# Optimization experiments

Measured on AMD Instinct MI355X. Metric: run time of the kernel, lower is better.

Reference implementation:

```python
import jax, jax.numpy as jnp
import numpy as np

B, C, H, W = 8, 192, 56, 56
OUT, K = 192, 9
BN_EPS = 1e-5


def _l2_normalize(x, axis):
    # matches torch F.normalize: x / max(||x||, eps)
    n = jnp.sqrt(jnp.sum(x * x, axis=axis, keepdims=True))
    return x / jnp.maximum(n, 1e-12)


def _knn_idx(x_bnc, k):
    # dense pairwise squared distances, then k nearest (includes self)
    sq = jnp.sum(x_bnc * x_bnc, axis=-1, keepdims=True)            # (b,n,1)
    dist = sq - 2.0 * jnp.einsum('bnc,bmc->bnm', x_bnc, x_bnc) + jnp.swapaxes(sq, 1, 2)
    _, idx = jax.lax.top_k(-dist, k)                                # (b,n,k)
    return idx


def setup_inputs() -> dict:
    key = jax.random.key(0)
    k1, k2 = jax.random.split(key)
    fan_in = 2 * C
    return {
        'x': jax.random.normal(k1, (B, C, H, W), dtype=jnp.float32),
        'conv_w': jax.random.normal(k2, (OUT, 2 * C), dtype=jnp.float32) * np.sqrt(2.0 / fan_in),
        'conv_b': jnp.zeros((OUT,), dtype=jnp.float32),
        'bn_gamma': jnp.ones((OUT,), dtype=jnp.float32),
        'bn_beta': jnp.zeros((OUT,), dtype=jnp.float32),
    }


def reference(x, conv_w, conv_b, bn_gamma, bn_beta):
    b, c, h, w = x.shape
    n = h * w
    xf = x.reshape(b, c, n)                      # (b,c,n) node features
    xt = jnp.swapaxes(xf, 1, 2)                  # (b,n,c)

    # graph build on L2-normalized features (torch does this under no_grad)
    xn = _l2_normalize(xt, axis=-1)
    idx = _knn_idx(jax.lax.stop_gradient(xn), K)  # (b,n,K) neighbor ids

    # gather neighbors; center gather is identity (center_idx == arange)
    x_j = jnp.take_along_axis(xt[:, :, None, :], idx[..., None], axis=1)  # (b,n,K,c)
    x_i = xt[:, :, None, :]                                               # (b,n,1,c)
    feat = jnp.concatenate([jnp.broadcast_to(x_i, x_j.shape), x_j - x_i], axis=-1)  # (b,n,K,2c)

    # 1x1 conv == per-edge linear
    y = jnp.einsum('bnke,oe->bnko', feat, conv_w) + conv_b                # (b,n,K,out)

    # BatchNorm2d (training-mode batch stats over b,n,K per channel)
    mean = jnp.mean(y, axis=(0, 1, 2))
    var = jnp.var(y, axis=(0, 1, 2))
    y = (y - mean) * jax.lax.rsqrt(var + BN_EPS) * bn_gamma + bn_beta

    y = jax.nn.gelu(y, approximate=False)
    y = jnp.max(y, axis=2)                        # max over K neighbors -> (b,n,out)
    return jnp.transpose(y, (0, 2, 1)).reshape(b, -1, h, w)
```

## Files before the change

kernel.cpp:

```cpp
#include <hip/hip_runtime.h>
#include <hip/hip_bf16.h>
#include <math.h>

#define BB 8
#define CC 192
#define HH 56
#define WW 56
#define NPTS 3136
#define OUTC 192
#define KNN 9
#define NTILES 49
#define NCH 2
#define NT4 98
#define NBLK4 (NT4 * BB)
#define K2BLKS (BB * NCH * NTILES)
#define K3BLKS ((BB * NPTS / 64) * 6)

typedef __bf16 bf16x8 __attribute__((ext_vector_type(8)));
typedef float  f32x16 __attribute__((ext_vector_type(16)));
typedef int    i32x4  __attribute__((ext_vector_type(4)));

__device__ __forceinline__ unsigned short f2bf(float f) {
    unsigned u = __float_as_uint(f);
    u += 0x7fffu + ((u >> 16) & 1u);
    return (unsigned short)(u >> 16);
}
__device__ __forceinline__ float bf2f(unsigned short h) {
    return __uint_as_float(((unsigned)h) << 16);
}
__device__ __forceinline__ float gelu_f(float z) {
    return 0.5f * z * (1.0f + erff(z * 0.70710678118654752f));
}

__device__ __forceinline__ void ins12u32(unsigned (&t)[12], unsigned key) {
    if (key >= t[11]) return;
    t[11] = key;
#pragma unroll
    for (int q = 11; q > 0; --q) {
        const unsigned a = t[q-1], bq = t[q];
        const bool sw = bq < a;
        t[q-1] = sw ? bq : a;
        t[q]   = sw ? a : bq;
    }
}

__device__ __forceinline__ void ins12u(unsigned long long (&t)[12], unsigned long long key) {
    if (key >= t[11]) return;
    t[11] = key;
#pragma unroll
    for (int q = 11; q > 0; --q) {
        const unsigned long long a = t[q-1], bq = t[q];
        const bool sw = bq < a;
        t[q-1] = sw ? bq : a;
        t[q]   = sw ? a : bq;
    }
}

__device__ __forceinline__ void ins9f(float (&d)[9], int (&ix)[9], float nd, int ni) {
    if (!((nd < d[8]) || (nd == d[8] && ni < ix[8]))) return;
    d[8] = nd; ix[8] = ni;
#pragma unroll
    for (int q = 8; q > 0; --q) {
        if ((d[q] < d[q-1]) || (d[q] == d[q-1] && ix[q] < ix[q-1])) {
            float t = d[q]; d[q] = d[q-1]; d[q-1] = t;
            int t2 = ix[q]; ix[q] = ix[q-1]; ix[q-1] = t2;
        }
    }
}

__global__ __launch_bounds__(256) void k1_normalize(const float* __restrict__ x,
                                                    float* __restrict__ xn,
                                                    unsigned short* __restrict__ xh,
                                                    unsigned short* __restrict__ xl,
                                                    float* __restrict__ normv,
                                                    float* __restrict__ sqv) {
    const int b  = blockIdx.y;
    const int n0 = blockIdx.x * 64;
    __shared__ float tile[64 * 193];
    __shared__ float red[4][64];
    __shared__ float inv[64];
    const int tid = threadIdx.x;
    const int p   = tid & 63;
    const int cg  = tid >> 6;
    const float* xb = x + (size_t)b * CC * NPTS;

    float acc = 0.f;
#pragma unroll 4
    for (int t = 0; t < 48; ++t) {
        const int c = cg * 48 + t;
        const float v = xb[(size_t)c * NPTS + n0 + p];
        tile[p * 193 + c] = v;
        acc += v * v;
    }
    red[cg][p] = acc;
    __syncthreads();
    if (cg == 0) {
        const float s  = red[0][p] + red[1][p] + red[2][p] + red[3][p];
        float nc = sqrtf(s);
        nc = fmaxf(nc, 1e-12f);
        normv[b * NPTS + n0 + p] = nc;
        const float iv = 1.0f / nc;
        inv[p] = iv;
        sqv[b * NPTS + n0 + p] = s * iv * iv;
    }
    __syncthreads();
    const size_t base = ((size_t)b * NPTS + n0) * CC;
    float* dst = xn + base;
    for (int q = tid; q < 64 * CC / 4; q += 256) {
        const int f   = q * 4;
        const int row = f / CC;
        const int c   = f - row * CC;
        const float iv = inv[row];
        float4 v;
        v.x = tile[row * 193 + c + 0] * iv;
        v.y = tile[row * 193 + c + 1] * iv;
        v.z = tile[row * 193 + c + 2] * iv;
        v.w = tile[row * 193 + c + 3] * iv;
        *(float4*)&dst[f] = v;
        ushort4 hv, lv;
        hv.x = f2bf(v.x); lv.x = f2bf(v.x - bf2f(hv.x));
        hv.y = f2bf(v.y); lv.y = f2bf(v.y - bf2f(hv.y));
        hv.z = f2bf(v.z); lv.z = f2bf(v.z - bf2f(hv.z));
        hv.w = f2bf(v.w); lv.w = f2bf(v.w - bf2f(hv.w));
        *(ushort4*)&xh[base + f] = hv;
        *(ushort4*)&xl[base + f] = lv;
    }
}

__global__ __launch_bounds__(256, 3) void k23_mega(const unsigned short* __restrict__ xh,
                                                   const unsigned short* __restrict__ xl,
                                                   unsigned long long* __restrict__ pd,
                                                   const unsigned short* __restrict__ wh,
                                                   const unsigned short* __restrict__ wl,
                                                   const float* __restrict__ normv,
                                                   const float* __restrict__ conv_b,
                                                   float* __restrict__ uv) {
    __shared__ __align__(16) char smem[51200];
    const int bid = blockIdx.x;
    const int tid = threadIdx.x;
    const int w    = tid >> 6;
    const int lane = tid & 63;
    const int l31  = lane & 31;
    const int lhi  = lane >> 5;
    const int koffe = lhi * 8;

    if (bid < K2BLKS) {
        const int b     = bid & 7;
        const int chunk = (bid >> 3) & 1;
        const int r0    = (bid >> 4) * 64;
        const int t0    = chunk ? 25 : 0;
        const int t1    = chunk ? 49 : 25;

        unsigned short* Cs  = (unsigned short*)smem;
        unsigned short* Rk1 = (unsigned short*)(smem + 25600);
        unsigned long long* cdu = (unsigned long long*)smem;

        const int wc   = w & 1;
        const int wr   = w >> 1;
        const int myrow = wc * 32 + l31;
        const int spnt = tid >> 2;
        const int sj   = tid & 3;

        const size_t rbase = ((size_t)b * NPTS + (r0 + myrow)) * CC;
        bf16x8 Rh0[6], Rl0[6];
#pragma unroll
        for (int c = 0; c < 6; ++c) {
            Rh0[c] = *(const bf16x8*)(const void*)(xh + rbase + c * 16 + koffe);
            Rl0[c] = *(const bf16x8*)(const void*)(xl + rbase + c * 16 + koffe);
        }

        {
            const size_t pb = ((size_t)b * NPTS + r0 + spnt) * CC + 96;
#pragma unroll
            for (int rep = 0; rep < 3; ++rep) {
                const int j = sj + rep * 4;
                *(uint4*)(void*)&Rk1[spnt * 200 + j * 8] =
                    *(const uint4*)(const void*)(xh + pb + j * 8);
            }
#pragma unroll
            for (int rep = 0; rep < 3; ++rep) {
                const int j = sj + rep * 4;
                *(uint4*)(void*)&Rk1[spnt * 200 + 96 + j * 8] =
                    *(const uint4*)(const void*)(xl + pb + j * 8);
            }
        }

        unsigned t12[12];
#pragma unroll
        for (int q = 0; q < 12; ++q) t12[q] = 0xFFFFFFFFu;

        const int cfb = (wr * 32 + l31) * 200 + koffe;
        const int rlb = myrow * 200 + koffe;

        for (int ct = t0; ct < t1; ++ct) {
            const int c0 = ct * 64;
            __syncthreads();
            {
                const size_t pb = ((size_t)b * NPTS + c0 + spnt) * CC;
#pragma unroll
                for (int rep = 0; rep < 6; ++rep) {
                    const int j = sj + rep * 4;
                    *(uint4*)(void*)&Cs[spnt * 200 + j * 8] =
                        *(const uint4*)(const void*)(xh + pb + j * 8);
                }
            }
            __syncthreads();

            f32x16 acc;
#pragma unroll
            for (int r = 0; r < 16; ++r) acc[r] = 0.f;

#pragma unroll
            for (int c = 0; c < 6; ++c) {
                const bf16x8 cf = *(const bf16x8*)(const void*)&Cs[cfb + c * 16];
                acc = __builtin_amdgcn_mfma_f32_32x32x16_bf16(cf, Rh0[c], acc, 0, 0, 0);
                acc = __builtin_amdgcn_mfma_f32_32x32x16_bf16(cf, Rl0[c], acc, 0, 0, 0);
            }
#pragma unroll
            for (int c = 0; c < 6; ++c) {
                const bf16x8 cf = *(const bf16x8*)(const void*)&Cs[cfb + (6 + c) * 16];
                const i32x4 th = *(const volatile i32x4*)(const volatile void*)&Rk1[rlb + c * 16];
                const i32x4 tl = *(const volatile i32x4*)(const volatile void*)&Rk1[rlb + 96 + c * 16];
                acc = __builtin_amdgcn_mfma_f32_32x32x16_bf16(cf, __builtin_bit_cast(bf16x8, th), acc, 0, 0, 0);
                acc = __builtin_amdgcn_mfma_f32_32x32x16_bf16(cf, __builtin_bit_cast(bf16x8, tl), acc, 0, 0, 0);
            }
            __syncthreads();
            {
                const size_t pb = ((size_t)b * NPTS + c0 + spnt) * CC;
#pragma unroll
                for (int rep = 0; rep < 6; ++rep) {
                    const int j = sj + rep * 4;
                    *(uint4*)(void*)&Cs[spnt * 200 + j * 8] =
                        *(const uint4*)(const void*)(xl + pb + j * 8);
                }
            }
            __syncthreads();
#pragma unroll
            for (int c = 0; c < 6; ++c) {
                const bf16x8 cl = *(const bf16x8*)(const void*)&Cs[cfb + c * 16];
                acc = __builtin_amdgcn_mfma_f32_32x32x16_bf16(cl, Rh0[c], acc, 0, 0, 0);
            }
#pragma unroll
            for (int c = 0; c < 6; ++c) {
                const bf16x8 cl = *(const bf16x8*)(const void*)&Cs[cfb + (6 + c) * 16];
                const i32x4 th = *(const volatile i32x4*)(const volatile void*)&Rk1[rlb + c * 16];
                acc = __builtin_amdgcn_mfma_f32_32x32x16_bf16(cl, __builtin_bit_cast(bf16x8, th), acc, 0, 0, 0);
            }

            const unsigned tbase = (unsigned)((ct - t0) << 4);
#pragma unroll
            for (int reg = 0; reg < 16; ++reg) {
                const float d = fmaxf(1.0f - acc[reg], 0.0f);
                const unsigned key = (__float_as_uint(d) & 0xFFFFFE00u) | (tbase | (unsigned)reg);
                ins12u32(t12, key);
            }
        }

        __syncthreads();
#pragma unroll
        for (int q = 0; q < 12; ++q) {
            const unsigned key = t12[q];
            const int tag = (int)(key & 511u);
            const int reg = tag & 15;
            const int col = (t0 + (tag >> 4)) * 64 + wr * 32 + ((reg & 3) + 8 * (reg >> 2) + 4 * lhi);
            cdu[(((wr * 2 + lhi) * 64) + myrow) * 12 + q] = ((unsigned long long)key << 32) | (unsigned)col;
        }
        __syncthreads();
        if (tid < 64) {
            unsigned long long t[12];
#pragma unroll
            for (int q = 0; q < 12; ++q) t[q] = cdu[tid * 12 + q];
            for (int s = 1; s < 4; ++s)
#pragma unroll
                for (int q = 0; q < 12; ++q) ins12u(t, cdu[(s * 64 + tid) * 12 + q]);
            const size_t gbase = ((size_t)b * NPTS + r0 + tid) * (NCH * 12) + chunk * 12;
#pragma unroll
            for (int q = 0; q < 12; ++q) pd[gbase + q] = t[q];
        }
    } else {
        const int id2 = bid - K2BLKS;
        const int ot  = id2 % 6;
        const int mt  = id2 / 6;
        const int m0  = mt * 64;
        const int o0  = ot * 64;
        const int wr  = w >> 1;
        const int wc  = w & 1;

        const size_t abase = (size_t)(m0 + wr * 32 + l31) * CC;
        bf16x8 Ah[12], Al[12];
#pragma unroll
        for (int c = 0; c < 12; ++c) {
            Ah[c] = *(const bf16x8*)(const void*)(xh + abase + c * 16 + koffe);
            Al[c] = *(const bf16x8*)(const void*)(xl + abase + c * 16 + koffe);
        }
        const int o = o0 + wc * 32 + l31;
        const unsigned short* whr = wh + (size_t)o * CC;
        const unsigned short* wlr = wl + (size_t)o * CC;

        f32x16 acc;
#pragma unroll
        for (int r = 0; r < 16; ++r) acc[r] = 0.f;
#pragma unroll
        for (int c = 0; c < 12; ++c) {
            const bf16x8 bh = *(const bf16x8*)(const void*)(whr + c * 16 + koffe);
            const bf16x8 bl = *(const bf16x8*)(const void*)(wlr + c * 16 + koffe);
            acc = __builtin_amdgcn_mfma_f32_32x32x16_bf16(Ah[c], bh, acc, 0, 0, 0);
            acc = __builtin_amdgcn_mfma_f32_32x32x16_bf16(Al[c], bh, acc, 0, 0, 0);
            acc = __builtin_amdgcn_mfma_f32_32x32x16_bf16(Ah[c], bl, acc, 0, 0, 0);
        }
        const float bias = (o < OUTC) ? conv_b[o] : 0.0f;
#pragma unroll
        for (int reg = 0; reg < 16; ++reg) {
            const int m = m0 + wr * 32 + (reg & 3) + 8 * (reg >> 2) + 4 * lhi;
            uv[(size_t)m * (2 * OUTC) + o] = acc[reg] * normv[m] + bias;
        }
    }
}

__global__ __launch_bounds__(128) void k2b_merge(const float* __restrict__ xn,
                                                 const float* __restrict__ sqv,
                                                 const unsigned long long* __restrict__ pd,
                                                 int* __restrict__ idxout) {
    const int b  = blockIdx.x;
    const int r0 = blockIdx.y * 32;
    __shared__ __align__(16) float xr_s[32][196];
    __shared__ int   ci[32][12];
    __shared__ float dd[32][13];
    __shared__ int   need[32];
    const int tid = threadIdx.x;
    const float* xb = xn + (size_t)b * NPTS * CC;

    for (int q = tid; q < 32 * 48; q += 128) {
        const int row = q / 48, c4 = q - row * 48;
        *(float4*)&xr_s[row][c4 * 4] = *(const float4*)&xb[(size_t)(r0 + row) * CC + c4 * 4];
    }
    if (tid < 32) {
        const size_t base = ((size_t)b * NPTS + r0 + tid) * (NCH * 12);
        unsigned long long t[12];
#pragma unroll
        for (int q = 0; q < 12; ++q) t[q] = pd[base + q];
        for (int s = 1; s < NCH; ++s)
#pragma unroll
            for (int q = 0; q < 12; ++q) ins12u(t, pd[base + s * 12 + q]);
#pragma unroll
        for (int q = 0; q < 12; ++q) ci[tid][q] = (int)(t[q] & 0xFFFFFFFFull);
        const float d9  = __uint_as_float((unsigned)(t[8] >> 32) & 0xFFFFFE00u);
        const float d10 = __uint_as_float((unsigned)(t[9] >> 32) & 0xFFFFFE00u);
        need[tid] = (d10 - d9) < 3e-4f ? 1 : 0;
    }
    __syncthreads();
    {
        const int p = tid >> 2;
        const int s = tid & 3;
        if (need[p]) {
            const float sqn = sqv[(size_t)b * NPTS + r0 + p];
#pragma unroll
            for (int t3 = 0; t3 < 3; ++t3) {
                const int cs2 = s + t3 * 4;
                const int m   = ci[p][cs2];
                const float* xm = xb + (size_t)m * CC;
                float4 a4 = make_float4(0.f, 0.f, 0.f, 0.f);
#pragma unroll 8
                for (int c4 = 0; c4 < 48; ++c4) {
                    const float4 xv = *(const float4*)&xm[c4 * 4];
                    const float4 rv = *(const float4*)&xr_s[p][c4 * 4];
                    a4.x += rv.x * xv.x;
                    a4.y += rv.y * xv.y;
                    a4.z += rv.z * xv.z;
                    a4.w += rv.w * xv.w;
                }
                const float dot = (a4.x + a4.y) + (a4.z + a4.w);
                dd[p][cs2] = sqn + sqv[(size_t)b * NPTS + m] - 2.0f * dot;
            }
        }
    }
    __syncthreads();
    if (tid < 32) {
        int* orow = &idxout[((size_t)b * NPTS + r0 + tid) * KNN];
        if (need[tid]) {
            float fd[9]; int fi[9];
#pragma unroll
            for (int q = 0; q < 9; ++q) { fd[q] = 3.4e38f; fi[q] = 0x7fffffff; }
#pragma unroll
            for (int cs2 = 0; cs2 < 12; ++cs2)
                ins9f(fd, fi, dd[tid][cs2], ci[tid][cs2]);
#pragma unroll
            for (int q = 0; q < 9; ++q) orow[q] = fi[q];
        } else {
#pragma unroll
            for (int q = 0; q < 9; ++q) orow[q] = ci[tid][q];
        }
    }
}

__global__ __launch_bounds__(256) void k3a_wcat(const float* __restrict__ cw,
                                               unsigned short* __restrict__ wh,
                                               unsigned short* __restrict__ wl) {
    const int i = blockIdx.x * 256 + threadIdx.x;
    if (i < 2 * OUTC * CC) {
        const int r = i / CC, c = i - r * CC;
        float val;
        if (r < OUTC) val = cw[r * (2 * CC) + c] - cw[r * (2 * CC) + CC + c];
        else          val = cw[(r - OUTC) * (2 * CC) + CC + c];
        const unsigned short h = f2bf(val);
        wh[i] = h;
        wl[i] = f2bf(val - bf2f(h));
    }
}

__global__ __launch_bounds__(256) void k4_fused(const float* __restrict__ uv,
                                                const int* __restrict__ idxb,
                                                float* __restrict__ amax,
                                                float* __restrict__ amin,
                                                float* __restrict__ partials) {
    const int flat = blockIdx.x;
    const int b    = flat & 7;
    const int tile = flat >> 3;
    const int tid  = threadIdx.x;
    const int p    = tid >> 3;
    const int g    = tid & 7;
    const int n    = tile * 32 + p;
    const size_t base = (size_t)b * NPTS;
    __shared__ float red[256 * 25];

    float sv[24], sv2[24], vmx[24], vmn[24];
#pragma unroll
    for (int c = 0; c < 24; ++c) { sv[c] = 0.f; sv2[c] = 0.f; vmx[c] = -3.4e38f; vmn[c] = 3.4e38f; }

    const int* ix = &idxb[(base + n) * KNN];
#pragma unroll
    for (int k = 0; k < KNN; ++k) {
        const int m = ix[k];
        const float* vr = &uv[(base + m) * (2 * OUTC) + OUTC + g * 24];
#pragma unroll
        for (int c4 = 0; c4 < 6; ++c4) {
            const float4 v = *(const float4*)&vr[c4 * 4];
            const int c = c4 * 4;
            sv[c+0] += v.x; sv2[c+0] += v.x*v.x; vmx[c+0] = fmaxf(vmx[c+0], v.x); vmn[c+0] = fminf(vmn[c+0], v.x);
            sv[c+1] += v.y; sv2[c+1] += v.y*v.y; vmx[c+1] = fmaxf(vmx[c+1], v.y); vmn[c+1] = fminf(vmn[c+1], v.y);
            sv[c+2] += v.z; sv2[c+2] += v.z*v.z; vmx[c+2] = fmaxf(vmx[c+2], v.z); vmn[c+2] = fminf(vmn[c+2], v.z);
            sv[c+3] += v.w; sv2[c+3] += v.w*v.w; vmx[c+3] = fmaxf(vmx[c+3], v.w); vmn[c+3] = fminf(vmn[c+3], v.w);
        }
    }
    const float* ur = &uv[(base + n) * (2 * OUTC) + g * 24];
    float S[24], Q[24];
    float* am = &amax[(base + n) * OUTC + g * 24];
    float* an = &amin[(base + n) * OUTC + g * 24];
#pragma unroll
    for (int c4 = 0; c4 < 6; ++c4) {
        const float4 u4 = *(const float4*)&ur[c4 * 4];
        const int c = c4 * 4;
        float4 mx, mn;
        mx.x = u4.x + vmx[c+0]; mn.x = u4.x + vmn[c+0];
        mx.y = u4.y + vmx[c+1]; mn.y = u4.y + vmn[c+1];
        mx.z = u4.z + vmx[c+2]; mn.z = u4.z + vmn[c+2];
        mx.w = u4.w + vmx[c+3]; mn.w = u4.w + vmn[c+3];
        *(float4*)&am[c4 * 4] = mx;
        *(float4*)&an[c4 * 4] = mn;
        S[c+0] = 9.f*u4.x + sv[c+0];  Q[c+0] = u4.x*(9.f*u4.x + 2.f*sv[c+0]) + sv2[c+0];
        S[c+1] = 9.f*u4.y + sv[c+1];  Q[c+1] = u4.y*(9.f*u4.y + 2.f*sv[c+1]) + sv2[c+1];
        S[c+2] = 9.f*u4.z + sv[c+2];  Q[c+2] = u4.z*(9.f*u4.z + 2.f*sv[c+2]) + sv2[c+2];
        S[c+3] = 9.f*u4.w + sv[c+3];  Q[c+3] = u4.w*(9.f*u4.w + 2.f*sv[c+3]) + sv2[c+3];
    }
#pragma unroll
    for (int c = 0; c < 24; ++c) red[tid * 25 + c] = S[c];
    __syncthreads();
    float accS = 0.f;
    if (tid < OUTC) {
        const int go = tid / 24, co = tid - go * 24;
        for (int pp = 0; pp < 32; ++pp) accS += red[(pp * 8 + go) * 25 + co];
    }
    __syncthreads();
#pragma unroll
    for (int c = 0; c < 24; ++c) red[tid * 25 + c] = Q[c];
    __syncthreads();
    if (tid < OUTC) {
        const int go = tid / 24, co = tid - go * 24;
        float accQ = 0.f;
        for (int pp = 0; pp < 32; ++pp) accQ += red[(pp * 8 + go) * 25 + co];
        partials[(size_t)flat * (2 * OUTC) + tid]        = accS;
        partials[(size_t)flat * (2 * OUTC) + OUTC + tid] = accQ;
    }
}

__global__ __launch_bounds__(256) void k4b_finalize(const float* __restrict__ partials,
                                                    const float* __restrict__ gamma,
                                                    const float* __restrict__ beta,
                                                    float* __restrict__ scsh) {
    const int o   = blockIdx.x;
    const int tid = threadIdx.x;
    __shared__ float sS[256], sQ[256];
    float S = 0.f, Q = 0.f;
    for (int blk = tid; blk < NBLK4; blk += 256) {
        S += partials[(size_t)blk * (2 * OUTC) + o];
        Q += partials[(size_t)blk * (2 * OUTC) + OUTC + o];
    }
    sS[tid] = S; sQ[tid] = Q;
    __syncthreads();
    for (int s = 128; s > 0; s >>= 1) {
        if (tid < s) { sS[tid] += sS[tid + s]; sQ[tid] += sQ[tid + s]; }
        __syncthreads();
    }
    if (tid == 0) {
        const float cnt  = (float)BB * (float)NPTS * (float)KNN;
        const float mean = sS[0] / cnt;
        float var = fmaxf(sQ[0] / cnt - mean * mean, 0.0f);
        const float scale = gamma[o] * rsqrtf(var + 1e-5f);
        scsh[o]        = scale;
        scsh[OUTC + o] = beta[o] - mean * scale;
    }
}

__global__ __launch_bounds__(256) void k5_out(const float* __restrict__ amax,
                                              const float* __restrict__ amin,
                                              const float* __restrict__ scsh,
                                              float* __restrict__ out) {
    const int b  = blockIdx.y;
    const int n0 = blockIdx.x * 64;
    __shared__ float zb[64 * 193];
    __shared__ float ssc[OUTC];
    __shared__ float ssh[OUTC];
    const int tid = threadIdx.x;
    for (int q = tid; q < OUTC; q += 256) {
        ssc[q] = scsh[q];
        ssh[q] = scsh[OUTC + q];
    }
    __syncthreads();
    const int p  = tid >> 2;
    const int og = tid & 3;
    const int n  = n0 + p;
    const size_t rb = ((size_t)b * NPTS + n) * OUTC + og * 48;
#pragma unroll
    for (int t4 = 0; t4 < 12; ++t4) {
        const float4 ax = *(const float4*)&amax[rb + t4 * 4];
        const float4 an = *(const float4*)&amin[rb + t4 * 4];
        const int ob = og * 48 + t4 * 4;
        float z1, z2;
        z1 = ax.x * ssc[ob+0] + ssh[ob+0]; z2 = an.x * ssc[ob+0] + ssh[ob+0];
        zb[p * 193 + ob + 0] = fmaxf(gelu_f(z1), gelu_f(z2));
        z1 = ax.y * ssc[ob+1] + ssh[ob+1]; z2 = an.y * ssc[ob+1] + ssh[ob+1];
        zb[p * 193 + ob + 1] = fmaxf(gelu_f(z1), gelu_f(z2));
        z1 = ax.z * ssc[ob+2] + ssh[ob+2]; z2 = an.z * ssc[ob+2] + ssh[ob+2];
        zb[p * 193 + ob + 2] = fmaxf(gelu_f(z1), gelu_f(z2));
        z1 = ax.w * ssc[ob+3] + ssh[ob+3]; z2 = an.w * ssc[ob+3] + ssh[ob+3];
        zb[p * 193 + ob + 3] = fmaxf(gelu_f(z1), gelu_f(z2));
    }
    __syncthreads();
    float* ob2 = out + (size_t)b * OUTC * NPTS;
    for (int q = tid; q < 64 * OUTC; q += 256) {
        const int o  = q >> 6;
        const int pp = q & 63;
        ob2[(size_t)o * NPTS + n0 + pp] = zb[pp * 193 + o];
    }
}

extern "C" void kernel_launch(void* const* d_in, const int* in_sizes, int n_in,
                              void* d_out, int out_size, void* d_ws, size_t ws_size,
                              hipStream_t stream) {
    const float* x        = (const float*)d_in[0];
    const float* conv_w   = (const float*)d_in[1];
    const float* conv_b   = (const float*)d_in[2];
    const float* bn_gamma = (const float*)d_in[3];
    const float* bn_beta  = (const float*)d_in[4];
    float* out = (float*)d_out;

    float* ws = (float*)d_ws;
    const size_t SZ_XN = (size_t)BB * NPTS * CC;
    const size_t SZ_NV = (size_t)BB * NPTS;
    const size_t SZ_A  = (size_t)BB * NPTS * OUTC;

    int*   idxb        = (int*)ws;
    unsigned short* wh = (unsigned short*)(idxb + (size_t)BB * NPTS * KNN);
    unsigned short* wl = wh + (size_t)(2 * OUTC) * CC;
    float* uv       = (float*)(wl + (size_t)(2 * OUTC) * CC);
    float* partials = uv + (size_t)BB * NPTS * (2 * OUTC);
    float* scsh     = partials + (size_t)NBLK4 * (2 * OUTC);
    float* normv    = scsh + 2 * OUTC;
    float* sqv      = normv + SZ_NV;
    float* xn       = sqv + SZ_NV;
    unsigned short* xh = (unsigned short*)(xn + SZ_XN);
    unsigned short* xl = xh + SZ_XN;
    unsigned long long* pd = (unsigned long long*)(xl + SZ_XN);
    float* amax = xn;
    float* amin = xn + SZ_A;

    k1_normalize<<<dim3(NTILES, BB), 256, 0, stream>>>(x, xn, xh, xl, normv, sqv);
    k3a_wcat<<<(2 * OUTC * CC + 255) / 256, 256, 0, stream>>>(conv_w, wh, wl);
    k23_mega<<<K2BLKS + K3BLKS, 256, 0, stream>>>(xh, xl, pd, wh, wl, normv, conv_b, uv);
    k2b_merge<<<dim3(BB, NT4), 128, 0, stream>>>(xn, sqv, pd, idxb);
    k4_fused<<<NBLK4, 256, 0, stream>>>(uv, idxb, amax, amin, partials);
    k4b_finalize<<<OUTC, 256, 0, stream>>>(partials, bn_gamma, bn_beta, scsh);
    k5_out<<<dim3(NTILES, BB), 256, 0, stream>>>(amax, amin, scsh, out);
}
```

Baseline: 349.7 us.

## Keep full row fragments in registers and prefetch next column tile

In the kNN distance phase, all 12 row-fragment chunks (hi and lo) now stay in registers instead of keeping half of them in a shared-memory staging area. This halves shared memory per block and drops the occupancy hint from launch bounds. The next column tile's hi/lo data is also prefetched into registers while the current tile's MFMAs run, so global load latency overlaps compute. The cost is much higher register pressure (about 48 extra VGPRs for the row fragments plus 48 for prefetch buffers), which may reduce occupancy or cause spills.

```diff
diff --git a/kernel.cpp b/kernel.cpp
--- a/kernel.cpp
+++ b/kernel.cpp
@@ -18,7 +18,6 @@
 
 typedef __bf16 bf16x8 __attribute__((ext_vector_type(8)));
 typedef float  f32x16 __attribute__((ext_vector_type(16)));
-typedef int    i32x4  __attribute__((ext_vector_type(4)));
 
 __device__ __forceinline__ unsigned short f2bf(float f) {
     unsigned u = __float_as_uint(f);
@@ -127,15 +126,15 @@
     }
 }
 
-__global__ __launch_bounds__(256, 3) void k23_mega(const unsigned short* __restrict__ xh,
-                                                   const unsigned short* __restrict__ xl,
-                                                   unsigned long long* __restrict__ pd,
-                                                   const unsigned short* __restrict__ wh,
-                                                   const unsigned short* __restrict__ wl,
-                                                   const float* __restrict__ normv,
-                                                   const float* __restrict__ conv_b,
-                                                   float* __restrict__ uv) {
-    __shared__ __align__(16) char smem[51200];
+__global__ __launch_bounds__(256) void k23_mega(const unsigned short* __restrict__ xh,
+                                                const unsigned short* __restrict__ xl,
+                                                unsigned long long* __restrict__ pd,
+                                                const unsigned short* __restrict__ wh,
+                                                const unsigned short* __restrict__ wl,
+                                                const float* __restrict__ normv,
+                                                const float* __restrict__ conv_b,
+                                                float* __restrict__ uv) {
+    __shared__ __align__(16) char smem[25600];
     const int bid = blockIdx.x;
     const int tid = threadIdx.x;
     const int w    = tid >> 6;
@@ -151,100 +150,79 @@
         const int t0    = chunk ? 25 : 0;
         const int t1    = chunk ? 49 : 25;
 
-        unsigned short* Cs  = (unsigned short*)smem;
-        unsigned short* Rk1 = (unsigned short*)(smem + 25600);
+        unsigned short* Cs = (unsigned short*)smem;
         unsigned long long* cdu = (unsigned long long*)smem;
 
-        const int wc   = w & 1;
-        const int wr   = w >> 1;
+        const int wc    = w & 1;
+        const int wr    = w >> 1;
         const int myrow = wc * 32 + l31;
-        const int spnt = tid >> 2;
-        const int sj   = tid & 3;
+        const int spnt  = tid >> 2;
+        const int sj    = tid & 3;
 
         const size_t rbase = ((size_t)b * NPTS + (r0 + myrow)) * CC;
-        bf16x8 Rh0[6], Rl0[6];
-#pragma unroll
-        for (int c = 0; c < 6; ++c) {
-            Rh0[c] = *(const bf16x8*)(const void*)(xh + rbase + c * 16 + koffe);
-            Rl0[c] = *(const bf16x8*)(const void*)(xl + rbase + c * 16 + koffe);
-        }
-
+        bf16x8 Rh[12], Rl[12];
+#pragma unroll
+        for (int c = 0; c < 12; ++c) {
+            Rh[c] = *(const bf16x8*)(const void*)(xh + rbase + c * 16 + koffe);
+            Rl[c] = *(const bf16x8*)(const void*)(xl + rbase + c * 16 + koffe);
+        }
+
+        unsigned t12[12];
+#pragma unroll
+        for (int q = 0; q < 12; ++q) t12[q] = 0xFFFFFFFFu;
+
+        const int cfb = (wr * 32 + l31) * 200 + koffe;
+
+        uint4 pfh[6], pfl[6];
         {
-            const size_t pb = ((size_t)b * NPTS + r0 + spnt) * CC + 96;
-#pragma unroll
-            for (int rep = 0; rep < 3; ++rep) {
+            const size_t pb = ((size_t)b * NPTS + t0 * 64 + spnt) * CC;
+#pragma unroll
+            for (int rep = 0; rep < 6; ++rep) {
                 const int j = sj + rep * 4;
-                *(uint4*)(void*)&Rk1[spnt * 200 + j * 8] =
-                    *(const uint4*)(const void*)(xh + pb + j * 8);
-            }
-#pragma unroll
-            for (int rep = 0; rep < 3; ++rep) {
-                const int j = sj + rep * 4;
-                *(uint4*)(void*)&Rk1[spnt * 200 + 96 + j * 8] =
-                    *(const uint4*)(const void*)(xl + pb + j * 8);
-            }
-        }
-
-        unsigned t12[12];
-#pragma unroll
-        for (int q = 0; q < 12; ++q) t12[q] = 0xFFFFFFFFu;
-
-        const int cfb = (wr * 32 + l31) * 200 + koffe;
-        const int rlb = myrow * 200 + koffe;
+                pfh[rep] = *(const uint4*)(const void*)(xh + pb + j * 8);
+                pfl[rep] = *(const uint4*)(const void*)(xl + pb + j * 8);
+            }
+        }
 
         for (int ct = t0; ct < t1; ++ct) {
-            const int c0 = ct * 64;
+            const size_t nb = ((size_t)b * NPTS + (ct + 1) * 64 + spnt) * CC;
+            const bool more = (ct + 1 < t1);
+
             __syncthreads();
-            {
-                const size_t pb = ((size_t)b * NPTS + c0 + spnt) * CC;
-#pragma unroll
-                for (int rep = 0; rep < 6; ++rep) {
-                    const int j = sj + rep * 4;
-                    *(uint4*)(void*)&Cs[spnt * 200 + j * 8] =
-                        *(const uint4*)(const void*)(xh + pb + j * 8);
-                }
-            }
+#pragma unroll
+            for (int rep = 0; rep < 6; ++rep)
+                *(uint4*)(void*)&Cs[spnt * 200 + (sj + rep * 4) * 8] = pfh[rep];
             __syncthreads();
+            if (more) {
+#pragma unroll
+                for (int rep = 0; rep < 6; ++rep)
+                    pfh[rep] = *(const uint4*)(const void*)(xh + nb + (sj + rep * 4) * 8);
+            }
 
             f32x16 acc;
 #pragma unroll
             for (int r = 0; r < 16; ++r) acc[r] = 0.f;
 
 #pragma unroll
-            for (int c = 0; c < 6; ++c) {
+            for (int c = 0; c < 12; ++c) {
                 const bf16x8 cf = *(const bf16x8*)(const void*)&Cs[cfb + c * 16];
-                acc = __builtin_amdgcn_mfma_f32_32x32x16_bf16(cf, Rh0[c], acc, 0, 0, 0);
-                acc = __builtin_amdgcn_mfma_f32_32x32x16_bf16(cf, Rl0[c], acc, 0, 0, 0);
-            }
-#pragma unroll
-            for (int c = 0; c < 6; ++c) {
-                const bf16x8 cf = *(const bf16x8*)(const void*)&Cs[cfb + (6 + c) * 16];
-                const i32x4 th = *(const volatile i32x4*)(const volatile void*)&Rk1[rlb + c * 16];
-                const i32x4 tl = *(const volatile i32x4*)(const volatile void*)&Rk1[rlb + 96 + c * 16];
-                acc = __builtin_amdgcn_mfma_f32_32x32x16_bf16(cf, __builtin_bit_cast(bf16x8, th), acc, 0, 0, 0);
-                acc = __builtin_amdgcn_mfma_f32_32x32x16_bf16(cf, __builtin_bit_cast(bf16x8, tl), acc, 0, 0, 0);
+                acc = __builtin_amdgcn_mfma_f32_32x32x16_bf16(cf, Rh[c], acc, 0, 0, 0);
+                acc = __builtin_amdgcn_mfma_f32_32x32x16_bf16(cf, Rl[c], acc, 0, 0, 0);
             }
             __syncthreads();
-            {
-                const size_t pb = ((size_t)b * NPTS + c0 + spnt) * CC;
-#pragma unroll
-                for (int rep = 0; rep < 6; ++rep) {
-                    const int j = sj + rep * 4;
-                    *(uint4*)(void*)&Cs[spnt * 200 + j * 8] =
-                        *(const uint4*)(const void*)(xl + pb + j * 8);
-                }
-            }
+#pragma unroll
+            for (int rep = 0; rep < 6; ++rep)
+                *(uint4*)(void*)&Cs[spnt * 200 + (sj + rep * 4) * 8] = pfl[rep];
             __syncthreads();
-#pragma unroll
-            for (int c = 0; c < 6; ++c) {
+            if (more) {
+#pragma unroll
+                for (int rep = 0; rep < 6; ++rep)
+                    pfl[rep] = *(const uint4*)(const void*)(xl + nb + (sj + rep * 4) * 8);
+            }
+#pragma unroll
+            for (int c = 0; c < 12; ++c) {
                 const bf16x8 cl = *(const bf16x8*)(const void*)&Cs[cfb + c * 16];
-                acc = __builtin_amdgcn_mfma_f32_32x32x16_bf16(cl, Rh0[c], acc, 0, 0, 0);
-            }
-#pragma unroll
-            for (int c = 0; c < 6; ++c) {
-                const bf16x8 cl = *(const bf16x8*)(const void*)&Cs[cfb + (6 + c) * 16];
-                const i32x4 th = *(const volatile i32x4*)(const volatile void*)&Rk1[rlb + c * 16];
-                acc = __builtin_amdgcn_mfma_f32_32x32x16_bf16(cl, __builtin_bit_cast(bf16x8, th), acc, 0, 0, 0);
+                acc = __builtin_amdgcn_mfma_f32_32x32x16_bf16(cl, Rh[c], acc, 0, 0, 0);
             }
 
             const unsigned tbase = (unsigned)((ct - t0) << 4);
```

New measurement: 526.4 us. +50.5%, slower.
